# Performance work log

Hardware: AMD Instinct MI355X
Metric: run time of the kernel (lower is better)

## Reference

```python
import jax, jax.numpy as jnp
import numpy as np

B, D, DFF, E, TOPK = 16384, 512, 2048, 8, 2


def setup_inputs() -> dict:
    key = jax.random.key(0)
    ks = jax.random.split(key, 5)
    scale_g = 1.0 / np.sqrt(D)
    scale_1 = 1.0 / np.sqrt(D)
    scale_2 = 1.0 / np.sqrt(DFF)
    return {
        "x": jax.random.normal(ks[0], (B, D), dtype=jnp.float32),
        "Wg": jax.random.normal(ks[1], (D, E), dtype=jnp.float32) * scale_g,
        "W1": jax.random.normal(ks[2], (E, D, DFF), dtype=jnp.float32) * scale_1,
        "b1": jnp.zeros((E, DFF), dtype=jnp.float32),
        "W2": jax.random.normal(ks[3], (E, DFF, D), dtype=jnp.float32) * scale_2,
        "b2": jnp.zeros((E, D), dtype=jnp.float32),
    }


def reference(x, Wg, W1, b1, W2, b2):
    # --- gate: top-k softmax routing weights, zeros elsewhere ---
    logits = x @ Wg                              # [B, E]
    probs = jax.nn.softmax(logits, axis=-1)      # [B, E]
    vals, idx = jax.lax.top_k(probs, TOPK)       # [B, K], [B, K]
    routing = jnp.zeros_like(probs).at[jnp.arange(x.shape[0])[:, None], idx].set(vals)  # [B, E]

    # --- experts: dense FFN per expert (equivalent math to masked dispatch) ---
    # original: gather selected tokens per expert, compute, scatter into
    # zeros[E, B, D], multiply by routing.T[:, :, None], sum over experts.
    # routing weight is exactly 0 for unselected tokens, so the dense form
    # out = sum_e routing[b, e] * expert_e(x_b) computes identical results.
    h = jax.nn.relu(jnp.einsum('bd,edf->ebf', x, W1) + b1[:, None, :])  # [E, B, DFF]
    y = jnp.einsum('ebf,efd->ebd', h, W2) + b2[:, None, :]              # [E, B, D]
    out = jnp.einsum('ebd,be->bd', y, routing)                          # [B, D]
    return out
```

## Files before the change

### kernel.cpp

```cpp
#include <hip/hip_runtime.h>
#include <stdint.h>

#define BTOK 16384
#define DM   512
#define DFF  2048
#define NE   8
#define NPAIR (BTOK*2)
#define MAXTA 24
#define MAXTB 48

typedef short s16x8 __attribute__((ext_vector_type(8)));
typedef float f32x4 __attribute__((ext_vector_type(4)));

__device__ __forceinline__ uint16_t f2b(float f) {
  uint32_t u = __float_as_uint(f);
  u += 0x7fff + ((u >> 16) & 1);
  return (uint16_t)(u >> 16);
}

__device__ __forceinline__ void g2l16(const void* gp, void* lp) {
  __builtin_amdgcn_global_load_lds(
      (__attribute__((address_space(1))) void*)(void*)gp,
      (__attribute__((address_space(3))) void*)lp, 16, 0, 0);
}

__global__ void k_tr(const float* __restrict__ w1, const float* __restrict__ w2,
                     uint16_t* __restrict__ w1t, uint16_t* __restrict__ w2t) {
  __shared__ float t[32][33];
  int z = blockIdx.z, bx = blockIdx.x;
  int R, C, c0, r0;
  const float* src;
  uint16_t* dst;
  if (z < 8) { R = DM; C = DFF; c0 = (bx & 63) * 32; r0 = (bx >> 6) * 32;
               src = w1 + (size_t)z * R * C; dst = w1t + (size_t)z * R * C; }
  else       { R = DFF; C = DM; c0 = (bx & 15) * 32; r0 = (bx >> 4) * 32;
               src = w2 + (size_t)(z - 8) * R * C; dst = w2t + (size_t)(z - 8) * R * C; }
  int tx = threadIdx.x, ty = threadIdx.y;
#pragma unroll
  for (int j = 0; j < 4; j++)
    t[ty + j * 8][tx] = src[(size_t)(r0 + ty + j * 8) * C + c0 + tx];
  __syncthreads();
#pragma unroll
  for (int j = 0; j < 4; j++)
    dst[(size_t)(c0 + ty + j * 8) * R + r0 + tx] = f2b(t[tx][ty + j * 8]);
}

__global__ __launch_bounds__(256) void k_route(const float* __restrict__ x,
                                               const float* __restrict__ wg,
                                               int* __restrict__ counts,
                                               int* __restrict__ tk_e, float* __restrict__ tk_w,
                                               uint16_t* __restrict__ xb) {
  __shared__ int hist[NE];
  int tid = threadIdx.x, lane = tid & 63, wave = tid >> 6;
  if (tid < NE) hist[tid] = 0;
  __syncthreads();

  float wv[8][8];
#pragma unroll
  for (int j = 0; j < 8; j++) {
    const float4* wr = (const float4*)(wg + (size_t)(j * 64 + lane) * NE);
    float4 a = wr[0], b = wr[1];
    wv[j][0] = a.x; wv[j][1] = a.y; wv[j][2] = a.z; wv[j][3] = a.w;
    wv[j][4] = b.x; wv[j][5] = b.y; wv[j][6] = b.z; wv[j][7] = b.w;
  }

  int tok0 = blockIdx.x * 64 + wave * 16;
  for (int tt = 0; tt < 16; tt++) {
    int tok = tok0 + tt;
    const float* xr = x + (size_t)tok * DM;
    float xv[8];
#pragma unroll
    for (int j = 0; j < 8; j++) xv[j] = xr[j * 64 + lane];
    float acc[NE];
#pragma unroll
    for (int e = 0; e < NE; e++) acc[e] = 0.f;
#pragma unroll
    for (int j = 0; j < 8; j++)
#pragma unroll
      for (int e = 0; e < NE; e++) acc[e] += xv[j] * wv[j][e];
#pragma unroll
    for (int e = 0; e < NE; e++) {
#pragma unroll
      for (int off = 32; off > 0; off >>= 1) acc[e] += __shfl_xor(acc[e], off, 64);
    }
    if (lane == 0) {
      float mx = acc[0];
      for (int e = 1; e < NE; e++) mx = fmaxf(mx, acc[e]);
      float p[NE], s = 0.f;
      for (int e = 0; e < NE; e++) { p[e] = __expf(acc[e] - mx); s += p[e]; }
      float inv = 1.f / s;
      int e0 = 0; float v0 = p[0];
      for (int e = 1; e < NE; e++) if (p[e] > v0) { v0 = p[e]; e0 = e; }
      int e1 = -1; float v1 = -1.f;
      for (int e = 0; e < NE; e++) if (e != e0 && p[e] > v1) { v1 = p[e]; e1 = e; }
      tk_e[tok * 2]     = e0; tk_w[tok * 2]     = v0 * inv;
      tk_e[tok * 2 + 1] = e1; tk_w[tok * 2 + 1] = v1 * inv;
      atomicAdd(&hist[e0], 1);
      atomicAdd(&hist[e1], 1);
    }
  }
  const float* xs = x + (size_t)blockIdx.x * 32768;
  uint16_t* xd = xb + (size_t)blockIdx.x * 32768;
#pragma unroll
  for (int i = 0; i < 16; i++) {
    int o = i * 2048 + tid * 8;
    float4 a = *(const float4*)(xs + o);
    float4 b = *(const float4*)(xs + o + 4);
    uint16_t v[8] = {f2b(a.x), f2b(a.y), f2b(a.z), f2b(a.w),
                     f2b(b.x), f2b(b.y), f2b(b.z), f2b(b.w)};
    *(s16x8*)(xd + o) = *(s16x8*)v;
  }
  __syncthreads();
  if (tid < NE) atomicAdd(&counts[tid], hist[tid]);
}

__global__ void k_setup(const int* __restrict__ counts, int* __restrict__ offsets,
                        int* __restrict__ trA, int* __restrict__ tcntA, int* __restrict__ tstartA,
                        int* __restrict__ trB, int* __restrict__ tcntB, int* __restrict__ tstartB) {
  if (threadIdx.x != 0 || blockIdx.x != 0) return;
  int off = 0;
  for (int e = 0; e < NE; e++) { offsets[e] = off; off += counts[e]; }
  offsets[NE] = off;
  int nt = 0;
  for (int e = 0; e < NE; e++) {
    tstartA[e] = nt; int c = 0;
    for (int r = offsets[e]; r < offsets[e + 1]; r += 256) { trA[nt++] = r; c++; }
    tcntA[e] = c;
  }
  int nb = 0;
  for (int e = 0; e < NE; e++) {
    tstartB[e] = nb; int c = 0;
    for (int r = offsets[e]; r < offsets[e + 1]; r += 128) { trB[nb++] = r; c++; }
    tcntB[e] = c;
  }
}

__global__ __launch_bounds__(256) void k_build(const int* __restrict__ tk_e, const float* __restrict__ tk_w,
                                               const int* __restrict__ offsets, int* __restrict__ cursors,
                                               int* __restrict__ tok_of, float* __restrict__ w_of,
                                               int* __restrict__ inv) {
  __shared__ int lcnt[NE], lbase[NE];
  int tid = threadIdx.x;
  int i = blockIdx.x * 256 + tid;
  if (tid < NE) lcnt[tid] = 0;
  __syncthreads();
  int e = tk_e[i];
  int local = atomicAdd(&lcnt[e], 1);
  __syncthreads();
  if (tid < NE) lbase[tid] = atomicAdd(&cursors[tid], lcnt[tid]);
  __syncthreads();
  int slot = offsets[e] + lbase[e] + local;
  tok_of[slot] = i >> 1;
  w_of[slot] = tk_w[i];
  inv[i] = slot;
}


#define LDS16(off) (*(const s16x8*)((const char*)smem + (off)))
#define VM8 asm volatile("s_waitcnt vmcnt(8)" ::: "memory")
#define VM4 asm volatile("s_waitcnt vmcnt(4)" ::: "memory")
#define VM0 asm volatile("s_waitcnt vmcnt(0)" ::: "memory")
#define NOVM do{}while(0)
#define NOSTG do{}while(0)
#define MFMA16 __builtin_amdgcn_mfma_f32_16x16x32_bf16

#define DS0_1(bb) do{ \
  bf0 = LDS16(offB0 + (bb)*32768); bf1 = LDS16(offB1 + (bb)*32768); \
  bf2 = LDS16(offB2 + (bb)*32768); bf3 = LDS16(offB3 + (bb)*32768); \
  af0 = LDS16(offA0 + (bb)*32768); af1 = LDS16(offA1 + (bb)*32768); \
  af2 = LDS16(offA2 + (bb)*32768); af3 = LDS16(offA3 + (bb)*32768); }while(0)
#define DS1_1(bb) do{ \
  af0 = LDS16(offA0 + (bb)*32768 + 4096); af1 = LDS16(offA1 + (bb)*32768 + 4096); \
  af2 = LDS16(offA2 + (bb)*32768 + 4096); af3 = LDS16(offA3 + (bb)*32768 + 4096); }while(0)
#define SA_1(bb) do{ \
  g2l16(gA0, (char*)smem + (bb)*32768 + wave*1024); \
  g2l16(gA1, (char*)smem + (bb)*32768 + 8192 + wave*1024); \
  gA0 += 32; gA1 += 32; }while(0)
#define SB_1(bb) do{ \
  g2l16(gB0, (char*)smem + (bb)*32768 + 16384 + wave*1024); \
  g2l16(gB1, (char*)smem + (bb)*32768 + 24576 + wave*1024); \
  gB0 += 32; gB1 += 32; }while(0)
#define MM16(H) do{ \
  __builtin_amdgcn_s_setprio(1); \
  acc[4*(H)+0][0] = MFMA16(af0, bf0, acc[4*(H)+0][0], 0, 0, 0); \
  acc[4*(H)+1][0] = MFMA16(af1, bf0, acc[4*(H)+1][0], 0, 0, 0); \
  acc[4*(H)+2][0] = MFMA16(af2, bf0, acc[4*(H)+2][0], 0, 0, 0); \
  acc[4*(H)+3][0] = MFMA16(af3, bf0, acc[4*(H)+3][0], 0, 0, 0); \
  acc[4*(H)+0][1] = MFMA16(af0, bf1, acc[4*(H)+0][1], 0, 0, 0); \
  acc[4*(H)+1][1] = MFMA16(af1, bf1, acc[4*(H)+1][1], 0, 0, 0); \
  acc[4*(H)+2][1] = MFMA16(af2, bf1, acc[4*(H)+2][1], 0, 0, 0); \
  acc[4*(H)+3][1] = MFMA16(af3, bf1, acc[4*(H)+3][1], 0, 0, 0); \
  acc[4*(H)+0][2] = MFMA16(af0, bf2, acc[4*(H)+0][2], 0, 0, 0); \
  acc[4*(H)+1][2] = MFMA16(af1, bf2, acc[4*(H)+1][2], 0, 0, 0); \
  acc[4*(H)+2][2] = MFMA16(af2, bf2, acc[4*(H)+2][2], 0, 0, 0); \
  acc[4*(H)+3][2] = MFMA16(af3, bf2, acc[4*(H)+3][2], 0, 0, 0); \
  acc[4*(H)+0][3] = MFMA16(af0, bf3, acc[4*(H)+0][3], 0, 0, 0); \
  acc[4*(H)+1][3] = MFMA16(af1, bf3, acc[4*(H)+1][3], 0, 0, 0); \
  acc[4*(H)+2][3] = MFMA16(af2, bf3, acc[4*(H)+2][3], 0, 0, 0); \
  acc[4*(H)+3][3] = MFMA16(af3, bf3, acc[4*(H)+3][3], 0, 0, 0); \
  __builtin_amdgcn_s_setprio(0); }while(0)
#define TILE1(bb, SA, SB, VMX) do{ \
  DS0_1(bb); SA; \
  __builtin_amdgcn_s_barrier(); \
  asm volatile("s_waitcnt lgkmcnt(0)" ::: "memory"); \
  MM16(0); \
  __builtin_amdgcn_s_barrier(); \
  DS1_1(bb); SB; \
  __builtin_amdgcn_s_barrier(); \
  asm volatile("s_waitcnt lgkmcnt(0)" ::: "memory"); \
  MM16(1); \
  VMX; \
  __builtin_amdgcn_s_barrier(); }while(0)

__global__ __launch_bounds__(512, 2) void k_gemm1(
    const uint16_t* __restrict__ xb, const uint16_t* __restrict__ w1t,
    const float* __restrict__ b1,
    const int* __restrict__ tok_of, const int* __restrict__ offsets,
    const int* __restrict__ trA, const int* __restrict__ tcntA, const int* __restrict__ tstartA,
    uint16_t* __restrict__ h) {
  __shared__ __align__(16) uint16_t smem[65536];
  int id = blockIdx.x;
  int e = id & 7, j = id >> 3;
  int ti = j >> 3;
  if (ti >= tcntA[e]) return;
  int row0 = trA[tstartA[e] + ti], end = offsets[e + 1];
  int n0 = (j & 7) * 256;
  int tid = threadIdx.x, lane = tid & 63, wave = tid >> 6;
  int wm = wave >> 2, wn = wave & 3;
  int l15 = lane & 15, l4 = lane >> 4;

  int offA0, offA1, offA2, offA3, offB0, offB1, offB2, offB3;
  { int r;
    r = wm*128 + 0*16 + l15; offA0 = r*64 + ((l4 ^ ((r>>1)&3)) << 4);
    r = wm*128 + 1*16 + l15; offA1 = r*64 + ((l4 ^ ((r>>1)&3)) << 4);
    r = wm*128 + 2*16 + l15; offA2 = r*64 + ((l4 ^ ((r>>1)&3)) << 4);
    r = wm*128 + 3*16 + l15; offA3 = r*64 + ((l4 ^ ((r>>1)&3)) << 4);
    r = wn*64  + 0*16 + l15; offB0 = 16384 + r*64 + ((l4 ^ ((r>>1)&3)) << 4);
    r = wn*64  + 1*16 + l15; offB1 = 16384 + r*64 + ((l4 ^ ((r>>1)&3)) << 4);
    r = wn*64  + 2*16 + l15; offB2 = 16384 + r*64 + ((l4 ^ ((r>>1)&3)) << 4);
    r = wn*64  + 3*16 + l15; offB3 = 16384 + r*64 + ((l4 ^ ((r>>1)&3)) << 4);
  }
  const uint16_t *gA0, *gA1, *gB0, *gB1;
  { int P = tid, r = P >> 2, c = (P & 3) ^ ((r >> 1) & 3);
    int s = row0 + r; if (s >= end) s = end - 1;
    gA0 = xb + (size_t)tok_of[s] * DM + c * 8;
    gB0 = w1t + (size_t)e * DFF * DM + (size_t)(n0 + r) * DM + c * 8; }
  { int P = 512 + tid, r = P >> 2, c = (P & 3) ^ ((r >> 1) & 3);
    int s = row0 + r; if (s >= end) s = end - 1;
    gA1 = xb + (size_t)tok_of[s] * DM + c * 8;
    gB1 = w1t + (size_t)e * DFF * DM + (size_t)(n0 + r) * DM + c * 8; }

  f32x4 acc[8][4];
#pragma unroll
  for (int m = 0; m < 8; m++)
#pragma unroll
    for (int n = 0; n < 4; n++)
#pragma unroll
      for (int i = 0; i < 4; i++) acc[m][n][i] = 0.f;

  s16x8 af0, af1, af2, af3, bf0, bf1, bf2, bf3;

  SA_1(0); SB_1(0); SA_1(1); SB_1(1); SA_1(2); SB_1(2);
  VM8;
  __builtin_amdgcn_s_barrier();

#pragma unroll 1
  for (int g = 0; g < 3; ++g) {
    TILE1(0, SA_1(3), SB_1(3), VM8);
    TILE1(1, SA_1(0), SB_1(0), VM8);
    TILE1(2, SA_1(1), SB_1(1), VM8);
    TILE1(3, SA_1(2), SB_1(2), VM8);
  }
  TILE1(0, SA_1(3), SB_1(3), VM8);
  TILE1(1, NOSTG, NOSTG, VM4);
  TILE1(2, NOSTG, NOSTG, VM0);
  TILE1(3, NOSTG, NOSTG, NOVM);

  {
    float bv[4];
#pragma unroll
    for (int n = 0; n < 4; n++) bv[n] = b1[(size_t)e * DFF + n0 + wn * 64 + n * 16 + l15];
    char* wrg = (char*)smem + wave * 2304;
    int rr = lane >> 2, cb = lane & 3;
#pragma unroll
    for (int m = 0; m < 8; m++) {
#pragma unroll
      for (int n = 0; n < 4; n++)
#pragma unroll
        for (int i = 0; i < 4; i++) {
          float v = fmaxf(acc[m][n][i] + bv[n], 0.f);
          *(uint16_t*)(wrg + (l4 * 4 + i) * 144 + (n * 16 + l15) * 2) = f2b(v);
        }
      int gr = row0 + wm * 128 + m * 16 + rr;
      const char* src = wrg + rr * 144 + cb * 32;
      if (gr < end) {
        uint16_t* dst = h + (size_t)gr * DFF + n0 + wn * 64 + cb * 16;
        *(s16x8*)dst       = *(const s16x8*)src;
        *(s16x8*)(dst + 8) = *(const s16x8*)(src + 16);
      }
    }
  }
}

__global__ __launch_bounds__(512, 2) void k_gemm2(
    const uint16_t* __restrict__ h, const uint16_t* __restrict__ w2t,
    const float* __restrict__ b2, const float* __restrict__ w_of,
    const int* __restrict__ offsets,
    const int* __restrict__ trA, const int* __restrict__ tcntA, const int* __restrict__ tstartA,
    float* __restrict__ y32) {
  __shared__ __align__(16) uint16_t smem[65536];
  int id = blockIdx.x;
  int e = id & 7, j = id >> 3;
  int ti = j >> 1;
  if (ti >= tcntA[e]) return;
  int row0 = trA[tstartA[e] + ti], end = offsets[e + 1];
  int n0 = (j & 1) * 256;
  int tid = threadIdx.x, lane = tid & 63, wave = tid >> 6;
  int wm = wave >> 2, wn = wave & 3;
  int l15 = lane & 15, l4 = lane >> 4;

  int offA0, offA1, offA2, offA3, offB0, offB1, offB2, offB3;
  { int r;
    r = wm*128 + 0*16 + l15; offA0 = r*64 + ((l4 ^ ((r>>1)&3)) << 4);
    r = wm*128 + 1*16 + l15; offA1 = r*64 + ((l4 ^ ((r>>1)&3)) << 4);
    r = wm*128 + 2*16 + l15; offA2 = r*64 + ((l4 ^ ((r>>1)&3)) << 4);
    r = wm*128 + 3*16 + l15; offA3 = r*64 + ((l4 ^ ((r>>1)&3)) << 4);
    r = wn*64  + 0*16 + l15; offB0 = 16384 + r*64 + ((l4 ^ ((r>>1)&3)) << 4);
    r = wn*64  + 1*16 + l15; offB1 = 16384 + r*64 + ((l4 ^ ((r>>1)&3)) << 4);
    r = wn*64  + 2*16 + l15; offB2 = 16384 + r*64 + ((l4 ^ ((r>>1)&3)) << 4);
    r = wn*64  + 3*16 + l15; offB3 = 16384 + r*64 + ((l4 ^ ((r>>1)&3)) << 4);
  }
  const uint16_t *gA0, *gA1, *gB0, *gB1;
  { int P = tid, r = P >> 2, c = (P & 3) ^ ((r >> 1) & 3);
    int s = row0 + r; if (s >= end) s = end - 1;
    gA0 = h + (size_t)s * DFF + c * 8;
    gB0 = w2t + (size_t)e * DM * DFF + (size_t)(n0 + r) * DFF + c * 8; }
  { int P = 512 + tid, r = P >> 2, c = (P & 3) ^ ((r >> 1) & 3);
    int s = row0 + r; if (s >= end) s = end - 1;
    gA1 = h + (size_t)s * DFF + c * 8;
    gB1 = w2t + (size_t)e * DM * DFF + (size_t)(n0 + r) * DFF + c * 8; }

  f32x4 acc[8][4];
#pragma unroll
  for (int m = 0; m < 8; m++)
#pragma unroll
    for (int n = 0; n < 4; n++)
#pragma unroll
      for (int i = 0; i < 4; i++) acc[m][n][i] = 0.f;

  s16x8 af0, af1, af2, af3, bf0, bf1, bf2, bf3;

  SA_1(0); SB_1(0); SA_1(1); SB_1(1); SA_1(2); SB_1(2);
  VM8;
  __builtin_amdgcn_s_barrier();

#pragma unroll 1
  for (int g = 0; g < 15; ++g) {
    TILE1(0, SA_1(3), SB_1(3), VM8);
    TILE1(1, SA_1(0), SB_1(0), VM8);
    TILE1(2, SA_1(1), SB_1(1), VM8);
    TILE1(3, SA_1(2), SB_1(2), VM8);
  }
  TILE1(0, SA_1(3), SB_1(3), VM8);
  TILE1(1, NOSTG, NOSTG, VM4);
  TILE1(2, NOSTG, NOSTG, VM0);
  TILE1(3, NOSTG, NOSTG, NOVM);

  {
    float bv[4];
#pragma unroll
    for (int n = 0; n < 4; n++) bv[n] = b2[(size_t)e * DM + n0 + wn * 64 + n * 16 + l15];
#pragma unroll
    for (int m = 0; m < 8; m++)
#pragma unroll
      for (int i = 0; i < 4; i++) {
        int slot = row0 + wm * 128 + m * 16 + l4 * 4 + i;
        if (slot < end) {
          float wgt = w_of[slot];
          size_t base = (size_t)slot * DM + n0 + wn * 64 + l15;
          y32[base +  0] = wgt * (acc[m][0][i] + bv[0]);
          y32[base + 16] = wgt * (acc[m][1][i] + bv[1]);
          y32[base + 32] = wgt * (acc[m][2][i] + bv[2]);
          y32[base + 48] = wgt * (acc[m][3][i] + bv[3]);
        }
      }
  }
}

__global__ __launch_bounds__(256) void k_combine(const float* __restrict__ y32,
                                                 const int* __restrict__ inv,
                                                 float* __restrict__ out) {
  int tid = threadIdx.x;
  int tok = blockIdx.x * 2 + (tid >> 7);
  int c4 = (tid & 127) * 4;
  int s0 = inv[tok * 2], s1 = inv[tok * 2 + 1];
  const float4 a = *(const float4*)(y32 + (size_t)s0 * DM + c4);
  const float4 b = *(const float4*)(y32 + (size_t)s1 * DM + c4);
  *(float4*)(out + (size_t)tok * DM + c4) = make_float4(a.x + b.x, a.y + b.y, a.z + b.z, a.w + b.w);
}

extern "C" void kernel_launch(void* const* d_in, const int* in_sizes, int n_in,
                              void* d_out, int out_size, void* d_ws, size_t ws_size,
                              hipStream_t stream) {
  const float* x  = (const float*)d_in[0];
  const float* wg = (const float*)d_in[1];
  const float* w1 = (const float*)d_in[2];
  const float* b1 = (const float*)d_in[3];
  const float* w2 = (const float*)d_in[4];
  const float* b2 = (const float*)d_in[5];
  float* out = (float*)d_out;

  char* ws = (char*)d_ws;
  const size_t MB = 1024 * 1024;
  uint16_t* xb   = (uint16_t*)ws;
  uint16_t* w1t  = (uint16_t*)(ws + 16 * MB);
  uint16_t* w2t  = (uint16_t*)(ws + 32 * MB);
  uint16_t* hbuf = (uint16_t*)(ws + 48 * MB);
  int* ctrl = (int*)(ws + 176 * MB);
  int*   counts  = ctrl;
  int*   cursors = ctrl + 8;
  int*   offsets = ctrl + 16;
  int*   tcntA   = ctrl + 32;
  int*   tstartA = ctrl + 40;
  int*   trA     = ctrl + 48;
  int*   tcntB   = ctrl + 240;
  int*   tstartB = ctrl + 248;
  int*   trB     = ctrl + 256;
  int*   tk_e    = ctrl + 1024;
  float* tk_w    = (float*)(ctrl + 1024 + 32768);
  int*   tok_of  = ctrl + 1024 + 2 * 32768;
  float* w_of    = (float*)(ctrl + 1024 + 3 * 32768);
  int*   inv     = ctrl + 1024 + 4 * 32768;
  float* y32     = (float*)(ws + 177 * MB);

  hipMemsetAsync(counts, 0, 16 * sizeof(int), stream);

  k_route<<<BTOK / 64, 256, 0, stream>>>(x, wg, counts, tk_e, tk_w, xb);
  k_tr<<<dim3(1024, 1, 16), dim3(32, 8), 0, stream>>>(w1, w2, w1t, w2t);
  k_setup<<<1, 64, 0, stream>>>(counts, offsets, trA, tcntA, tstartA, trB, tcntB, tstartB);
  k_build<<<NPAIR / 256, 256, 0, stream>>>(tk_e, tk_w, offsets, cursors, tok_of, w_of, inv);
  k_gemm1<<<NE * 8 * MAXTA, 512, 0, stream>>>(xb, w1t, b1, tok_of, offsets,
                                              trA, tcntA, tstartA, hbuf);
  k_gemm2<<<NE * 2 * MAXTA, 512, 0, stream>>>(hbuf, w2t, b2, w_of, offsets,
                                              trA, tcntA, tstartA, y32);
  k_combine<<<BTOK / 2, 256, 0, stream>>>(y32, inv, out);
}
```

Before: 396.2 us.

## Shrink GEMM tiles to 128x256 with flat tile list and triple-buffered LDS

Both expert GEMMs now use 128-row by 256-column tiles with 256 threads per block, 4 waves by 2 split, and a 4x8 MFMA accumulator per wave, replacing 256x256 tiles with 512 threads. The K-loop moves from four LDS buffers to three, which lowers shared memory per block. The setup kernel now emits one flat list of (row, expert) tiles, so launched blocks map to real tiles instead of a fixed per-expert grid where many exit early. The aim is less padding waste on partial expert tiles and better CU load balance. The cost is lower arithmetic intensity per tile and more total blocks and weight reloads.

```diff
diff --git a/kernel.cpp b/kernel.cpp
--- a/kernel.cpp
+++ b/kernel.cpp
@@ -6,8 +6,7 @@
 #define DFF  2048
 #define NE   8
 #define NPAIR (BTOK*2)
-#define MAXTA 24
-#define MAXTB 48
+#define MAXT 288
 
 typedef short s16x8 __attribute__((ext_vector_type(8)));
 typedef float f32x4 __attribute__((ext_vector_type(4)));
@@ -115,24 +114,15 @@
 }
 
 __global__ void k_setup(const int* __restrict__ counts, int* __restrict__ offsets,
-                        int* __restrict__ trA, int* __restrict__ tcntA, int* __restrict__ tstartA,
-                        int* __restrict__ trB, int* __restrict__ tcntB, int* __restrict__ tstartB) {
+                        int* __restrict__ trB, int* __restrict__ texp, int* __restrict__ ntB) {
   if (threadIdx.x != 0 || blockIdx.x != 0) return;
   int off = 0;
   for (int e = 0; e < NE; e++) { offsets[e] = off; off += counts[e]; }
   offsets[NE] = off;
   int nt = 0;
-  for (int e = 0; e < NE; e++) {
-    tstartA[e] = nt; int c = 0;
-    for (int r = offsets[e]; r < offsets[e + 1]; r += 256) { trA[nt++] = r; c++; }
-    tcntA[e] = c;
-  }
-  int nb = 0;
-  for (int e = 0; e < NE; e++) {
-    tstartB[e] = nb; int c = 0;
-    for (int r = offsets[e]; r < offsets[e + 1]; r += 128) { trB[nb++] = r; c++; }
-    tcntB[e] = c;
-  }
+  for (int e = 0; e < NE; e++)
+    for (int r = offsets[e]; r < offsets[e + 1]; r += 128) { trB[nt] = r; texp[nt] = e; nt++; }
+  *ntB = nt;
 }
 
 __global__ __launch_bounds__(256) void k_build(const int* __restrict__ tk_e, const float* __restrict__ tk_w,
@@ -157,231 +147,235 @@
 
 
 #define LDS16(off) (*(const s16x8*)((const char*)smem + (off)))
-#define VM8 asm volatile("s_waitcnt vmcnt(8)" ::: "memory")
-#define VM4 asm volatile("s_waitcnt vmcnt(4)" ::: "memory")
+#define VM6 asm volatile("s_waitcnt vmcnt(6)" ::: "memory")
 #define VM0 asm volatile("s_waitcnt vmcnt(0)" ::: "memory")
 #define NOVM do{}while(0)
 #define NOSTG do{}while(0)
 #define MFMA16 __builtin_amdgcn_mfma_f32_16x16x32_bf16
-
-#define DS0_1(bb) do{ \
-  bf0 = LDS16(offB0 + (bb)*32768); bf1 = LDS16(offB1 + (bb)*32768); \
-  bf2 = LDS16(offB2 + (bb)*32768); bf3 = LDS16(offB3 + (bb)*32768); \
-  af0 = LDS16(offA0 + (bb)*32768); af1 = LDS16(offA1 + (bb)*32768); \
-  af2 = LDS16(offA2 + (bb)*32768); af3 = LDS16(offA3 + (bb)*32768); }while(0)
-#define DS1_1(bb) do{ \
-  af0 = LDS16(offA0 + (bb)*32768 + 4096); af1 = LDS16(offA1 + (bb)*32768 + 4096); \
-  af2 = LDS16(offA2 + (bb)*32768 + 4096); af3 = LDS16(offA3 + (bb)*32768 + 4096); }while(0)
-#define SA_1(bb) do{ \
-  g2l16(gA0, (char*)smem + (bb)*32768 + wave*1024); \
-  g2l16(gA1, (char*)smem + (bb)*32768 + 8192 + wave*1024); \
+#define BSTR 24576
+
+#define DS0_P(bb) do{ \
+  bf0 = LDS16(offB0 + (bb)*BSTR); bf1 = LDS16(offB1 + (bb)*BSTR); \
+  bf2 = LDS16(offB2 + (bb)*BSTR); bf3 = LDS16(offB3 + (bb)*BSTR); \
+  bf4 = LDS16(offB4 + (bb)*BSTR); bf5 = LDS16(offB5 + (bb)*BSTR); \
+  bf6 = LDS16(offB6 + (bb)*BSTR); bf7 = LDS16(offB7 + (bb)*BSTR); \
+  af0 = LDS16(offA0 + (bb)*BSTR); af1 = LDS16(offA1 + (bb)*BSTR); }while(0)
+#define DS1_P(bb) do{ \
+  af2 = LDS16(offA2 + (bb)*BSTR); af3 = LDS16(offA3 + (bb)*BSTR); }while(0)
+#define SA_P(bb) do{ \
+  g2l16(gA0, (char*)smem + (bb)*BSTR + wave*1024); \
+  g2l16(gA1, (char*)smem + (bb)*BSTR + 4096 + wave*1024); \
   gA0 += 32; gA1 += 32; }while(0)
-#define SB_1(bb) do{ \
-  g2l16(gB0, (char*)smem + (bb)*32768 + 16384 + wave*1024); \
-  g2l16(gB1, (char*)smem + (bb)*32768 + 24576 + wave*1024); \
-  gB0 += 32; gB1 += 32; }while(0)
-#define MM16(H) do{ \
+#define SB_P(bb) do{ \
+  g2l16(gB0, (char*)smem + (bb)*BSTR + 8192 + wave*1024); \
+  g2l16(gB1, (char*)smem + (bb)*BSTR + 12288 + wave*1024); \
+  g2l16(gB2, (char*)smem + (bb)*BSTR + 16384 + wave*1024); \
+  g2l16(gB3, (char*)smem + (bb)*BSTR + 20480 + wave*1024); \
+  gB0 += 32; gB1 += 32; gB2 += 32; gB3 += 32; }while(0)
+#define MM16A do{ \
   __builtin_amdgcn_s_setprio(1); \
-  acc[4*(H)+0][0] = MFMA16(af0, bf0, acc[4*(H)+0][0], 0, 0, 0); \
-  acc[4*(H)+1][0] = MFMA16(af1, bf0, acc[4*(H)+1][0], 0, 0, 0); \
-  acc[4*(H)+2][0] = MFMA16(af2, bf0, acc[4*(H)+2][0], 0, 0, 0); \
-  acc[4*(H)+3][0] = MFMA16(af3, bf0, acc[4*(H)+3][0], 0, 0, 0); \
-  acc[4*(H)+0][1] = MFMA16(af0, bf1, acc[4*(H)+0][1], 0, 0, 0); \
-  acc[4*(H)+1][1] = MFMA16(af1, bf1, acc[4*(H)+1][1], 0, 0, 0); \
-  acc[4*(H)+2][1] = MFMA16(af2, bf1, acc[4*(H)+2][1], 0, 0, 0); \
-  acc[4*(H)+3][1] = MFMA16(af3, bf1, acc[4*(H)+3][1], 0, 0, 0); \
-  acc[4*(H)+0][2] = MFMA16(af0, bf2, acc[4*(H)+0][2], 0, 0, 0); \
-  acc[4*(H)+1][2] = MFMA16(af1, bf2, acc[4*(H)+1][2], 0, 0, 0); \
-  acc[4*(H)+2][2] = MFMA16(af2, bf2, acc[4*(H)+2][2], 0, 0, 0); \
-  acc[4*(H)+3][2] = MFMA16(af3, bf2, acc[4*(H)+3][2], 0, 0, 0); \
-  acc[4*(H)+0][3] = MFMA16(af0, bf3, acc[4*(H)+0][3], 0, 0, 0); \
-  acc[4*(H)+1][3] = MFMA16(af1, bf3, acc[4*(H)+1][3], 0, 0, 0); \
-  acc[4*(H)+2][3] = MFMA16(af2, bf3, acc[4*(H)+2][3], 0, 0, 0); \
-  acc[4*(H)+3][3] = MFMA16(af3, bf3, acc[4*(H)+3][3], 0, 0, 0); \
+  acc[0][0] = MFMA16(af0, bf0, acc[0][0], 0, 0, 0); \
+  acc[1][0] = MFMA16(af1, bf0, acc[1][0], 0, 0, 0); \
+  acc[0][1] = MFMA16(af0, bf1, acc[0][1], 0, 0, 0); \
+  acc[1][1] = MFMA16(af1, bf1, acc[1][1], 0, 0, 0); \
+  acc[0][2] = MFMA16(af0, bf2, acc[0][2], 0, 0, 0); \
+  acc[1][2] = MFMA16(af1, bf2, acc[1][2], 0, 0, 0); \
+  acc[0][3] = MFMA16(af0, bf3, acc[0][3], 0, 0, 0); \
+  acc[1][3] = MFMA16(af1, bf3, acc[1][3], 0, 0, 0); \
+  acc[0][4] = MFMA16(af0, bf4, acc[0][4], 0, 0, 0); \
+  acc[1][4] = MFMA16(af1, bf4, acc[1][4], 0, 0, 0); \
+  acc[0][5] = MFMA16(af0, bf5, acc[0][5], 0, 0, 0); \
+  acc[1][5] = MFMA16(af1, bf5, acc[1][5], 0, 0, 0); \
+  acc[0][6] = MFMA16(af0, bf6, acc[0][6], 0, 0, 0); \
+  acc[1][6] = MFMA16(af1, bf6, acc[1][6], 0, 0, 0); \
+  acc[0][7] = MFMA16(af0, bf7, acc[0][7], 0, 0, 0); \
+  acc[1][7] = MFMA16(af1, bf7, acc[1][7], 0, 0, 0); \
   __builtin_amdgcn_s_setprio(0); }while(0)
-#define TILE1(bb, SA, SB, VMX) do{ \
-  DS0_1(bb); SA; \
+#define MM16B do{ \
+  __builtin_amdgcn_s_setprio(1); \
+  acc[2][0] = MFMA16(af2, bf0, acc[2][0], 0, 0, 0); \
+  acc[3][0] = MFMA16(af3, bf0, acc[3][0], 0, 0, 0); \
+  acc[2][1] = MFMA16(af2, bf1, acc[2][1], 0, 0, 0); \
+  acc[3][1] = MFMA16(af3, bf1, acc[3][1], 0, 0, 0); \
+  acc[2][2] = MFMA16(af2, bf2, acc[2][2], 0, 0, 0); \
+  acc[3][2] = MFMA16(af3, bf2, acc[3][2], 0, 0, 0); \
+  acc[2][3] = MFMA16(af2, bf3, acc[2][3], 0, 0, 0); \
+  acc[3][3] = MFMA16(af3, bf3, acc[3][3], 0, 0, 0); \
+  acc[2][4] = MFMA16(af2, bf4, acc[2][4], 0, 0, 0); \
+  acc[3][4] = MFMA16(af3, bf4, acc[3][4], 0, 0, 0); \
+  acc[2][5] = MFMA16(af2, bf5, acc[2][5], 0, 0, 0); \
+  acc[3][5] = MFMA16(af3, bf5, acc[3][5], 0, 0, 0); \
+  acc[2][6] = MFMA16(af2, bf6, acc[2][6], 0, 0, 0); \
+  acc[3][6] = MFMA16(af3, bf6, acc[3][6], 0, 0, 0); \
+  acc[2][7] = MFMA16(af2, bf7, acc[2][7], 0, 0, 0); \
+  acc[3][7] = MFMA16(af3, bf7, acc[3][7], 0, 0, 0); \
+  __builtin_amdgcn_s_setprio(0); }while(0)
+#define TILEP(bb, SA, SB, VMX) do{ \
+  DS0_P(bb); SA; \
   __builtin_amdgcn_s_barrier(); \
   asm volatile("s_waitcnt lgkmcnt(0)" ::: "memory"); \
-  MM16(0); \
+  MM16A; \
   __builtin_amdgcn_s_barrier(); \
-  DS1_1(bb); SB; \
+  DS1_P(bb); SB; \
   __builtin_amdgcn_s_barrier(); \
   asm volatile("s_waitcnt lgkmcnt(0)" ::: "memory"); \
-  MM16(1); \
+  MM16B; \
   VMX; \
   __builtin_amdgcn_s_barrier(); }while(0)
 
-__global__ __launch_bounds__(512, 2) void k_gemm1(
+#define GEOM_SETUP \
+  int tid = threadIdx.x, lane = tid & 63, wave = tid >> 6; \
+  int wm = wave >> 1, wn = wave & 1; \
+  int l15 = lane & 15, l4 = lane >> 4; \
+  int offA0, offA1, offA2, offA3; \
+  int offB0, offB1, offB2, offB3, offB4, offB5, offB6, offB7; \
+  { int r; \
+    r = wm*64 + 0*16 + l15; offA0 = r*64 + ((l4 ^ ((r>>1)&3)) << 4); \
+    r = wm*64 + 1*16 + l15; offA1 = r*64 + ((l4 ^ ((r>>1)&3)) << 4); \
+    r = wm*64 + 2*16 + l15; offA2 = r*64 + ((l4 ^ ((r>>1)&3)) << 4); \
+    r = wm*64 + 3*16 + l15; offA3 = r*64 + ((l4 ^ ((r>>1)&3)) << 4); \
+    r = wn*128 + 0*16 + l15; offB0 = 8192 + r*64 + ((l4 ^ ((r>>1)&3)) << 4); \
+    r = wn*128 + 1*16 + l15; offB1 = 8192 + r*64 + ((l4 ^ ((r>>1)&3)) << 4); \
+    r = wn*128 + 2*16 + l15; offB2 = 8192 + r*64 + ((l4 ^ ((r>>1)&3)) << 4); \
+    r = wn*128 + 3*16 + l15; offB3 = 8192 + r*64 + ((l4 ^ ((r>>1)&3)) << 4); \
+    r = wn*128 + 4*16 + l15; offB4 = 8192 + r*64 + ((l4 ^ ((r>>1)&3)) << 4); \
+    r = wn*128 + 5*16 + l15; offB5 = 8192 + r*64 + ((l4 ^ ((r>>1)&3)) << 4); \
+    r = wn*128 + 6*16 + l15; offB6 = 8192 + r*64 + ((l4 ^ ((r>>1)&3)) << 4); \
+    r = wn*128 + 7*16 + l15; offB7 = 8192 + r*64 + ((l4 ^ ((r>>1)&3)) << 4); \
+  } \
+  int rp = tid >> 2, cp = (tid & 3) ^ ((rp >> 1) & 3);
+
+#define ACC_INIT \
+  f32x4 acc[4][8]; \
+  _Pragma("unroll") for (int m = 0; m < 4; m++) \
+  _Pragma("unroll") for (int n = 0; n < 8; n++) \
+  _Pragma("unroll") for (int i = 0; i < 4; i++) acc[m][n][i] = 0.f; \
+  s16x8 af0, af1, af2, af3, bf0, bf1, bf2, bf3, bf4, bf5, bf6, bf7;
+
+__global__ __launch_bounds__(256, 2) void k_gemm1(
     const uint16_t* __restrict__ xb, const uint16_t* __restrict__ w1t,
     const float* __restrict__ b1,
     const int* __restrict__ tok_of, const int* __restrict__ offsets,
-    const int* __restrict__ trA, const int* __restrict__ tcntA, const int* __restrict__ tstartA,
+    const int* __restrict__ trB, const int* __restrict__ texp, const int* __restrict__ ntB,
     uint16_t* __restrict__ h) {
-  __shared__ __align__(16) uint16_t smem[65536];
+  __shared__ __align__(16) uint16_t smem[36864];
   int id = blockIdx.x;
-  int e = id & 7, j = id >> 3;
-  int ti = j >> 3;
-  if (ti >= tcntA[e]) return;
-  int row0 = trA[tstartA[e] + ti], end = offsets[e + 1];
-  int n0 = (j & 7) * 256;
-  int tid = threadIdx.x, lane = tid & 63, wave = tid >> 6;
-  int wm = wave >> 2, wn = wave & 3;
-  int l15 = lane & 15, l4 = lane >> 4;
-
-  int offA0, offA1, offA2, offA3, offB0, offB1, offB2, offB3;
-  { int r;
-    r = wm*128 + 0*16 + l15; offA0 = r*64 + ((l4 ^ ((r>>1)&3)) << 4);
-    r = wm*128 + 1*16 + l15; offA1 = r*64 + ((l4 ^ ((r>>1)&3)) << 4);
-    r = wm*128 + 2*16 + l15; offA2 = r*64 + ((l4 ^ ((r>>1)&3)) << 4);
-    r = wm*128 + 3*16 + l15; offA3 = r*64 + ((l4 ^ ((r>>1)&3)) << 4);
-    r = wn*64  + 0*16 + l15; offB0 = 16384 + r*64 + ((l4 ^ ((r>>1)&3)) << 4);
-    r = wn*64  + 1*16 + l15; offB1 = 16384 + r*64 + ((l4 ^ ((r>>1)&3)) << 4);
-    r = wn*64  + 2*16 + l15; offB2 = 16384 + r*64 + ((l4 ^ ((r>>1)&3)) << 4);
-    r = wn*64  + 3*16 + l15; offB3 = 16384 + r*64 + ((l4 ^ ((r>>1)&3)) << 4);
-  }
-  const uint16_t *gA0, *gA1, *gB0, *gB1;
-  { int P = tid, r = P >> 2, c = (P & 3) ^ ((r >> 1) & 3);
-    int s = row0 + r; if (s >= end) s = end - 1;
-    gA0 = xb + (size_t)tok_of[s] * DM + c * 8;
-    gB0 = w1t + (size_t)e * DFF * DM + (size_t)(n0 + r) * DM + c * 8; }
-  { int P = 512 + tid, r = P >> 2, c = (P & 3) ^ ((r >> 1) & 3);
-    int s = row0 + r; if (s >= end) s = end - 1;
-    gA1 = xb + (size_t)tok_of[s] * DM + c * 8;
-    gB1 = w1t + (size_t)e * DFF * DM + (size_t)(n0 + r) * DM + c * 8; }
-
-  f32x4 acc[8][4];
-#pragma unroll
-  for (int m = 0; m < 8; m++)
-#pragma unroll
-    for (int n = 0; n < 4; n++)
-#pragma unroll
-      for (int i = 0; i < 4; i++) acc[m][n][i] = 0.f;
-
-  s16x8 af0, af1, af2, af3, bf0, bf1, bf2, bf3;
-
-  SA_1(0); SB_1(0); SA_1(1); SB_1(1); SA_1(2); SB_1(2);
-  VM8;
+  int tile = id >> 3, n0 = (id & 7) * 256;
+  if (tile >= *ntB) return;
+  int e = texp[tile], row0 = trB[tile], end = offsets[e + 1];
+  GEOM_SETUP;
+
+  const uint16_t *gA0, *gA1, *gB0, *gB1, *gB2, *gB3;
+  { int s0 = row0 + rp;      if (s0 >= end) s0 = end - 1;
+    int s1 = row0 + rp + 64; if (s1 >= end) s1 = end - 1;
+    gA0 = xb + (size_t)tok_of[s0] * DM + cp * 8;
+    gA1 = xb + (size_t)tok_of[s1] * DM + cp * 8; }
+  { const uint16_t* wb = w1t + (size_t)e * DFF * DM;
+    gB0 = wb + (size_t)(n0 + rp +   0) * DM + cp * 8;
+    gB1 = wb + (size_t)(n0 + rp +  64) * DM + cp * 8;
+    gB2 = wb + (size_t)(n0 + rp + 128) * DM + cp * 8;
+    gB3 = wb + (size_t)(n0 + rp + 192) * DM + cp * 8; }
+
+  ACC_INIT;
+
+  SA_P(0); SB_P(0); SA_P(1); SB_P(1);
+  VM6;
   __builtin_amdgcn_s_barrier();
 
 #pragma unroll 1
-  for (int g = 0; g < 3; ++g) {
-    TILE1(0, SA_1(3), SB_1(3), VM8);
-    TILE1(1, SA_1(0), SB_1(0), VM8);
-    TILE1(2, SA_1(1), SB_1(1), VM8);
-    TILE1(3, SA_1(2), SB_1(2), VM8);
-  }
-  TILE1(0, SA_1(3), SB_1(3), VM8);
-  TILE1(1, NOSTG, NOSTG, VM4);
-  TILE1(2, NOSTG, NOSTG, VM0);
-  TILE1(3, NOSTG, NOSTG, NOVM);
+  for (int g = 0; g < 4; ++g) {
+    TILEP(0, SA_P(2), SB_P(2), VM6);
+    TILEP(1, SA_P(0), SB_P(0), VM6);
+    TILEP(2, SA_P(1), SB_P(1), VM6);
+  }
+  TILEP(0, SA_P(2), SB_P(2), VM6);
+  TILEP(1, SA_P(0), SB_P(0), VM6);
+  TILEP(2, NOSTG, NOSTG, VM0);
+  TILEP(0, NOSTG, NOSTG, NOVM);
 
   {
-    float bv[4];
-#pragma unroll
-    for (int n = 0; n < 4; n++) bv[n] = b1[(size_t)e * DFF + n0 + wn * 64 + n * 16 + l15];
-    char* wrg = (char*)smem + wave * 2304;
+    float bv[8];
+#pragma unroll
+    for (int n = 0; n < 8; n++) bv[n] = b1[(size_t)e * DFF + n0 + wn * 128 + n * 16 + l15];
+    char* wrg = (char*)smem + wave * 4608;
     int rr = lane >> 2, cb = lane & 3;
 #pragma unroll
-    for (int m = 0; m < 8; m++) {
-#pragma unroll
-      for (int n = 0; n < 4; n++)
+    for (int m = 0; m < 4; m++) {
+#pragma unroll
+      for (int n = 0; n < 8; n++)
 #pragma unroll
         for (int i = 0; i < 4; i++) {
           float v = fmaxf(acc[m][n][i] + bv[n], 0.f);
-          *(uint16_t*)(wrg + (l4 * 4 + i) * 144 + (n * 16 + l15) * 2) = f2b(v);
+          *(uint16_t*)(wrg + (l4 * 4 + i) * 272 + (n * 16 + l15) * 2) = f2b(v);
         }
-      int gr = row0 + wm * 128 + m * 16 + rr;
-      const char* src = wrg + rr * 144 + cb * 32;
+      int gr = row0 + wm * 64 + m * 16 + rr;
+      const char* src = wrg + rr * 272 + cb * 64;
       if (gr < end) {
-        uint16_t* dst = h + (size_t)gr * DFF + n0 + wn * 64 + cb * 16;
-        *(s16x8*)dst       = *(const s16x8*)src;
-        *(s16x8*)(dst + 8) = *(const s16x8*)(src + 16);
+        uint16_t* dst = h + (size_t)gr * DFF + n0 + wn * 128 + cb * 32;
+        *(s16x8*)(dst +  0) = *(const s16x8*)(src +  0);
+        *(s16x8*)(dst +  8) = *(const s16x8*)(src + 16);
+        *(s16x8*)(dst + 16) = *(const s16x8*)(src + 32);
+        *(s16x8*)(dst + 24) = *(const s16x8*)(src + 48);
       }
     }
   }
 }
 
-__global__ __launch_bounds__(512, 2) void k_gemm2(
+__global__ __launch_bounds__(256, 2) void k_gemm2(
     const uint16_t* __restrict__ h, const uint16_t* __restrict__ w2t,
     const float* __restrict__ b2, const float* __restrict__ w_of,
     const int* __restrict__ offsets,
-    const int* __restrict__ trA, const int* __restrict__ tcntA, const int* __restrict__ tstartA,
+    const int* __restrict__ trB, const int* __restrict__ texp, const int* __restrict__ ntB,
     float* __restrict__ y32) {
-  __shared__ __align__(16) uint16_t smem[65536];
+  __shared__ __align__(16) uint16_t smem[36864];
   int id = blockIdx.x;
-  int e = id & 7, j = id >> 3;
-  int ti = j >> 1;
-  if (ti >= tcntA[e]) return;
-  int row0 = trA[tstartA[e] + ti], end = offsets[e + 1];
-  int n0 = (j & 1) * 256;
-  int tid = threadIdx.x, lane = tid & 63, wave = tid >> 6;
-  int wm = wave >> 2, wn = wave & 3;
-  int l15 = lane & 15, l4 = lane >> 4;
-
-  int offA0, offA1, offA2, offA3, offB0, offB1, offB2, offB3;
-  { int r;
-    r = wm*128 + 0*16 + l15; offA0 = r*64 + ((l4 ^ ((r>>1)&3)) << 4);
-    r = wm*128 + 1*16 + l15; offA1 = r*64 + ((l4 ^ ((r>>1)&3)) << 4);
-    r = wm*128 + 2*16 + l15; offA2 = r*64 + ((l4 ^ ((r>>1)&3)) << 4);
-    r = wm*128 + 3*16 + l15; offA3 = r*64 + ((l4 ^ ((r>>1)&3)) << 4);
-    r = wn*64  + 0*16 + l15; offB0 = 16384 + r*64 + ((l4 ^ ((r>>1)&3)) << 4);
-    r = wn*64  + 1*16 + l15; offB1 = 16384 + r*64 + ((l4 ^ ((r>>1)&3)) << 4);
-    r = wn*64  + 2*16 + l15; offB2 = 16384 + r*64 + ((l4 ^ ((r>>1)&3)) << 4);
-    r = wn*64  + 3*16 + l15; offB3 = 16384 + r*64 + ((l4 ^ ((r>>1)&3)) << 4);
-  }
-  const uint16_t *gA0, *gA1, *gB0, *gB1;
-  { int P = tid, r = P >> 2, c = (P & 3) ^ ((r >> 1) & 3);
-    int s = row0 + r; if (s >= end) s = end - 1;
-    gA0 = h + (size_t)s * DFF + c * 8;
-    gB0 = w2t + (size_t)e * DM * DFF + (size_t)(n0 + r) * DFF + c * 8; }
-  { int P = 512 + tid, r = P >> 2, c = (P & 3) ^ ((r >> 1) & 3);
-    int s = row0 + r; if (s >= end) s = end - 1;
-    gA1 = h + (size_t)s * DFF + c * 8;
-    gB1 = w2t + (size_t)e * DM * DFF + (size_t)(n0 + r) * DFF + c * 8; }
-
-  f32x4 acc[8][4];
-#pragma unroll
-  for (int m = 0; m < 8; m++)
-#pragma unroll
-    for (int n = 0; n < 4; n++)
-#pragma unroll
-      for (int i = 0; i < 4; i++) acc[m][n][i] = 0.f;
-
-  s16x8 af0, af1, af2, af3, bf0, bf1, bf2, bf3;
-
-  SA_1(0); SB_1(0); SA_1(1); SB_1(1); SA_1(2); SB_1(2);
-  VM8;
+  int tile = id >> 1, n0 = (id & 1) * 256;
+  if (tile >= *ntB) return;
+  int e = texp[tile], row0 = trB[tile], end = offsets[e + 1];
+  GEOM_SETUP;
+
+  const uint16_t *gA0, *gA1, *gB0, *gB1, *gB2, *gB3;
+  { int s0 = row0 + rp;      if (s0 >= end) s0 = end - 1;
+    int s1 = row0 + rp + 64; if (s1 >= end) s1 = end - 1;
+    gA0 = h + (size_t)s0 * DFF + cp * 8;
+    gA1 = h + (size_t)s1 * DFF + cp * 8; }
+  { const uint16_t* wb = w2t + (size_t)e * DM * DFF;
+    gB0 = wb + (size_t)(n0 + rp +   0) * DFF + cp * 8;
+    gB1 = wb + (size_t)(n0 + rp +  64) * DFF + cp * 8;
+    gB2 = wb + (size_t)(n0 + rp + 128) * DFF + cp * 8;
+    gB3 = wb + (size_t)(n0 + rp + 192) * DFF + cp * 8; }
+
+  ACC_INIT;
+
+  SA_P(0); SB_P(0); SA_P(1); SB_P(1);
+  VM6;
   __builtin_amdgcn_s_barrier();
 
 #pragma unroll 1
-  for (int g = 0; g < 15; ++g) {
-    TILE1(0, SA_1(3), SB_1(3), VM8);
-    TILE1(1, SA_1(0), SB_1(0), VM8);
-    TILE1(2, SA_1(1), SB_1(1), VM8);
-    TILE1(3, SA_1(2), SB_1(2), VM8);
-  }
-  TILE1(0, SA_1(3), SB_1(3), VM8);
-  TILE1(1, NOSTG, NOSTG, VM4);
-  TILE1(2, NOSTG, NOSTG, VM0);
-  TILE1(3, NOSTG, NOSTG, NOVM);
+  for (int g = 0; g < 20; ++g) {
+    TILEP(0, SA_P(2), SB_P(2), VM6);
+    TILEP(1, SA_P(0), SB_P(0), VM6);
+    TILEP(2, SA_P(1), SB_P(1), VM6);
+  }
+  TILEP(0, SA_P(2), SB_P(2), VM6);
+  TILEP(1, SA_P(0), SB_P(0), VM6);
+  TILEP(2, NOSTG, NOSTG, VM0);
+  TILEP(0, NOSTG, NOSTG, NOVM);
 
   {
-    float bv[4];
-#pragma unroll
-    for (int n = 0; n < 4; n++) bv[n] = b2[(size_t)e * DM + n0 + wn * 64 + n * 16 + l15];
-#pragma unroll
-    for (int m = 0; m < 8; m++)
+    float bv[8];
+#pragma unroll
+    for (int n = 0; n < 8; n++) bv[n] = b2[(size_t)e * DM + n0 + wn * 128 + n * 16 + l15];
+#pragma unroll
+    for (int m = 0; m < 4; m++)
 #pragma unroll
       for (int i = 0; i < 4; i++) {
-        int slot = row0 + wm * 128 + m * 16 + l4 * 4 + i;
+        int slot = row0 + wm * 64 + m * 16 + l4 * 4 + i;
         if (slot < end) {
           float wgt = w_of[slot];
-          size_t base = (size_t)slot * DM + n0 + wn * 64 + l15;
-          y32[base +  0] = wgt * (acc[m][0][i] + bv[0]);
-          y32[base + 16] = wgt * (acc[m][1][i] + bv[1]);
-          y32[base + 32] = wgt * (acc[m][2][i] + bv[2]);
-          y32[base + 48] = wgt * (acc[m][3][i] + bv[3]);
+          size_t base = (size_t)slot * DM + n0 + wn * 128 + l15;
+#pragma unroll
+          for (int n = 0; n < 8; n++) y32[base + n * 16] = wgt * (acc[m][n][i] + bv[n]);
         }
       }
   }
@@ -420,12 +414,9 @@
   int*   counts  = ctrl;
   int*   cursors = ctrl + 8;
   int*   offsets = ctrl + 16;
-  int*   tcntA   = ctrl + 32;
-  int*   tstartA = ctrl + 40;
-  int*   trA     = ctrl + 48;
-  int*   tcntB   = ctrl + 240;
-  int*   tstartB = ctrl + 248;
-  int*   trB     = ctrl + 256;
+  int*   ntB     = ctrl + 32;
+  int*   trB     = ctrl + 64;
+  int*   texp    = ctrl + 384;
   int*   tk_e    = ctrl + 1024;
   float* tk_w    = (float*)(ctrl + 1024 + 32768);
   int*   tok_of  = ctrl + 1024 + 2 * 32768;
@@ -437,11 +428,11 @@
 
   k_route<<<BTOK / 64, 256, 0, stream>>>(x, wg, counts, tk_e, tk_w, xb);
   k_tr<<<dim3(1024, 1, 16), dim3(32, 8), 0, stream>>>(w1, w2, w1t, w2t);
-  k_setup<<<1, 64, 0, stream>>>(counts, offsets, trA, tcntA, tstartA, trB, tcntB, tstartB);
+  k_setup<<<1, 64, 0, stream>>>(counts, offsets, trB, texp, ntB);
   k_build<<<NPAIR / 256, 256, 0, stream>>>(tk_e, tk_w, offsets, cursors, tok_of, w_of, inv);
-  k_gemm1<<<NE * 8 * MAXTA, 512, 0, stream>>>(xb, w1t, b1, tok_of, offsets,
-                                              trA, tcntA, tstartA, hbuf);
-  k_gemm2<<<NE * 2 * MAXTA, 512, 0, stream>>>(hbuf, w2t, b2, w_of, offsets,
-                                              trA, tcntA, tstartA, y32);
+  k_gemm1<<<MAXT * 8, 256, 0, stream>>>(xb, w1t, b1, tok_of, offsets,
+                                        trB, texp, ntB, hbuf);
+  k_gemm2<<<MAXT * 2, 256, 0, stream>>>(hbuf, w2t, b2, w_of, offsets,
+                                        trB, texp, ntB, y32);
   k_combine<<<BTOK / 2, 256, 0, stream>>>(y32, inv, out);
 }
```

After: 391.7 us. Within noise of the previous version (-1.1%).
